# Kernel optimization log

Measured on AMD Instinct MI355X. Metric: run time of the kernel, lower is better.

## Reference

```python
import jax, jax.numpy as jnp
import numpy as np

NUM_ANCHORS = 3
NUM_CLASS = 7
IMG_SIZE = 608.0


def setup_inputs() -> dict:
    key = jax.random.key(0)
    k1, k2 = jax.random.split(key)
    B, A, G = 32, NUM_ANCHORS, 152
    C = 7 + NUM_CLASS  # per-anchor channels
    x = jax.random.normal(k1, (B, A * C, G, G), dtype=jnp.float32)
    # anchor (w, h) priors in pixels
    anchors = jnp.array([[38.0, 84.0], [110.0, 45.0], [170.0, 160.0]], dtype=jnp.float32)
    return {"x": x, "anchors": anchors}


def _decode(x, anchors):
    B, AC, G, _ = x.shape
    A = NUM_ANCHORS
    C = AC // A  # 14
    # [B, A, G, G, C]
    y = x.reshape(B, A, C, G, G).transpose(0, 1, 3, 4, 2)

    off_x = jax.nn.sigmoid(y[..., 0])
    off_y = jax.nn.sigmoid(y[..., 1])
    scale_w = jnp.exp(y[..., 2])
    scale_h = jnp.exp(y[..., 3])
    im = y[..., 4]
    re = y[..., 5]
    conf = jax.nn.sigmoid(y[..., 6])
    cls = y[..., 7:]  # [B, A, G, G, num_class]

    # grid_x[gy, gx] = gx ; grid_y = grid_x.T
    grid = jnp.arange(G, dtype=jnp.float32)
    grid_x = grid[None, :]  # broadcasts over rows
    grid_y = grid[:, None]
    stride = IMG_SIZE / G

    anchor_x = jnp.floor((off_x + grid_x) * stride)
    anchor_y = jnp.floor((off_y + grid_y) * stride)
    anchor_yaw = jnp.arctan(im / re)
    anchor_w = scale_w * anchors[None, :, 0, None, None]
    anchor_h = scale_h * anchors[None, :, 1, None, None]

    # classes: [B, A, G, G, nc] -> [B, A, nc, G, G] -> [B, A*nc, G, G]
    cls_flat = cls.transpose(0, 1, 4, 2, 3).reshape(B, A * NUM_CLASS, G, G)

    # channel concat exactly as torch.cat(..., dim=1): 8 fields of A channels + A*nc class channels
    feats = jnp.concatenate(
        [im, re, anchor_yaw, conf, anchor_x, anchor_y, anchor_w, anchor_h, cls_flat],
        axis=1,
    )  # [B, 15*A, G, G]
    # faithful to .view(B, 15, A, G, G).permute(0, 2, 3, 4, 1).view(B, A*G*G, 15)
    pred = feats.reshape(B, 15, A, G, G).transpose(0, 2, 3, 4, 1).reshape(B, A * G * G, 15)
    return pred


def reference(x, anchors):
    return _decode(x, anchors)
```

## Files before the change

kernel.cpp:

```cpp
#include <hip/hip_runtime.h>


constexpr int G   = 152;
constexpr int GG  = G * G;
constexpr int Cc  = 14;
constexpr int NTHREADS  = 256;
constexpr int TILE_ROWS = 1024;

typedef float f32x4 __attribute__((ext_vector_type(4)));

__device__ __forceinline__ float sigmoidf_(float v) {
    return 1.0f / (1.0f + __expf(-v));
}

__global__ __launch_bounds__(NTHREADS) void decode_kernel(
    const float* __restrict__ x, const float* __restrict__ anchors,
    float* __restrict__ out, int total_rows)
{
    __shared__ f32x4 lds4[TILE_ROWS * 15 / 4];

    const int t  = threadIdx.x;
    const int r0 = blockIdx.x * TILE_ROWS + t * 4;

    if (r0 + 3 < total_rows) {
        const unsigned ba = (unsigned)r0 / (unsigned)GG;
        const int s0      = r0 - (int)ba * GG;
        const unsigned b  = ba / 3u;
        const int a2      = (int)(ba - b * 3u);
        const int gy      = s0 / G;
        const int gx0     = s0 - gy * G;

        const float an_w = anchors[a2 * 2 + 0];
        const float an_h = anchors[a2 * 2 + 1];

        const float* xb = x + (size_t)(b * 42u) * GG + s0;
        const int cb = a2 * Cc;

        const f32x4 vtx = *(const f32x4*)(xb + (size_t)(cb + 0) * GG);
        const f32x4 vty = *(const f32x4*)(xb + (size_t)(cb + 1) * GG);
        const f32x4 vtw = *(const f32x4*)(xb + (size_t)(cb + 2) * GG);
        const f32x4 vth = *(const f32x4*)(xb + (size_t)(cb + 3) * GG);
        const f32x4 vim = *(const f32x4*)(xb + (size_t)(cb + 4) * GG);
        const f32x4 vre = *(const f32x4*)(xb + (size_t)(cb + 5) * GG);
        const f32x4 vcf = *(const f32x4*)(xb + (size_t)(cb + 6) * GG);
        f32x4 vcls[7];
#pragma unroll
        for (int fc = 0; fc < 7; ++fc) {
            const int cc = fc * 3 + a2;
            const int as = cc / 7;
            const int k  = cc - as * 7;
            vcls[fc] = *(const f32x4*)(xb + (size_t)(as * Cc + 7 + k) * GG);
        }

        float v[60];
#pragma unroll
        for (int u = 0; u < 4; ++u) {
            const float im  = vim[u];
            const float re  = vre[u];
            const float yaw = atanf(im / re);
            const float cf  = sigmoidf_(vcf[u]);
            const float ax  = floorf((sigmoidf_(vtx[u]) + (float)(gx0 + u)) * 4.0f);
            const float ay  = floorf((sigmoidf_(vty[u]) + (float)gy) * 4.0f);
            const float aw  = __expf(vtw[u]) * an_w;
            const float ah  = __expf(vth[u]) * an_h;
            v[u * 15 + 0] = im;  v[u * 15 + 1] = re;
            v[u * 15 + 2] = yaw; v[u * 15 + 3] = cf;
            v[u * 15 + 4] = ax;  v[u * 15 + 5] = ay;
            v[u * 15 + 6] = aw;  v[u * 15 + 7] = ah;
#pragma unroll
            for (int fc = 0; fc < 7; ++fc) v[u * 15 + 8 + fc] = vcls[fc][u];
        }
#pragma unroll
        for (int j = 0; j < 15; ++j) {
            f32x4 q = { v[4 * j], v[4 * j + 1], v[4 * j + 2], v[4 * j + 3] };
            lds4[15 * t + j] = q;
        }
    }
    __syncthreads();

    const long long block_word0 = (long long)blockIdx.x * (TILE_ROWS * 15);
    const long long total_words = (long long)total_rows * 15;
    float* outp = out + block_word0;
#pragma unroll
    for (int i = 0; i < 15; ++i) {
        const int gr = i * NTHREADS + t;
        if (block_word0 + 4 * gr + 3 < total_words) {
            f32x4 q = lds4[gr];
            *(f32x4*)(outp + 4 * gr) = q;
        }
    }
}

extern "C" void kernel_launch(void* const* d_in, const int* in_sizes, int n_in,
                              void* d_out, int out_size, void* d_ws, size_t ws_size,
                              hipStream_t stream) {
    const float* x       = (const float*)d_in[0];
    const float* anchors = (const float*)d_in[1];
    float* out           = (float*)d_out;

    const int B          = in_sizes[0] / (3 * Cc * GG);
    const int total_rows = B * 3 * GG;
    const int nblocks    = (total_rows + TILE_ROWS - 1) / TILE_ROWS;

    hipLaunchKernelGGL(decode_kernel, dim3(nblocks), dim3(NTHREADS), 0, stream,
                       x, anchors, out, total_rows);
}
```

Baseline: 43.59 us.

## Process one row per thread with per-wave LDS staging and wave barrier

Each thread now handles one output row with scalar loads instead of four rows with vector loads. Each wave writes its own 240-float4 slice of a smaller LDS tile and syncs with a wave barrier instead of a block barrier. Launch bounds ask for 8 blocks per SM, and bounds checks are dropped on the assumption that total rows divide evenly by 256. The aim is higher occupancy and less block-level synchronisation, at the cost of narrower global loads and many more blocks.

```diff
diff --git a/kernel.cpp b/kernel.cpp
--- a/kernel.cpp
+++ b/kernel.cpp
@@ -4,8 +4,7 @@
 constexpr int G   = 152;
 constexpr int GG  = G * G;
 constexpr int Cc  = 14;
-constexpr int NTHREADS  = 256;
-constexpr int TILE_ROWS = 1024;
+constexpr int NTHREADS = 256;
 
 typedef float f32x4 __attribute__((ext_vector_type(4)));
 
@@ -13,78 +12,67 @@
     return 1.0f / (1.0f + __expf(-v));
 }
 
-__global__ __launch_bounds__(NTHREADS) void decode_kernel(
+__global__ __launch_bounds__(NTHREADS, 8) void decode_kernel(
     const float* __restrict__ x, const float* __restrict__ anchors,
-    float* __restrict__ out, int total_rows)
+    float* __restrict__ out)
 {
-    __shared__ f32x4 lds4[TILE_ROWS * 15 / 4];
+    __shared__ f32x4 lds4[NTHREADS * 15 / 4];
+    float* ldsf = (float*)lds4;
 
-    const int t  = threadIdx.x;
-    const int r0 = blockIdx.x * TILE_ROWS + t * 4;
+    const int t = threadIdx.x;
+    const int w = t >> 6;
+    const int l = t & 63;
+    const int r = blockIdx.x * NTHREADS + t;
 
-    if (r0 + 3 < total_rows) {
-        const unsigned ba = (unsigned)r0 / (unsigned)GG;
-        const int s0      = r0 - (int)ba * GG;
-        const unsigned b  = ba / 3u;
-        const int a2      = (int)(ba - b * 3u);
-        const int gy      = s0 / G;
-        const int gx0     = s0 - gy * G;
+    const unsigned ba = (unsigned)r / (unsigned)GG;
+    const int s       = r - (int)ba * GG;
+    const unsigned b  = ba / 3u;
+    const int a2      = (int)(ba - b * 3u);
+    const int gy      = s / G;
+    const int gx      = s - gy * G;
 
-        const float an_w = anchors[a2 * 2 + 0];
-        const float an_h = anchors[a2 * 2 + 1];
+    const float an_w = anchors[a2 * 2 + 0];
+    const float an_h = anchors[a2 * 2 + 1];
 
-        const float* xb = x + (size_t)(b * 42u) * GG + s0;
-        const int cb = a2 * Cc;
+    const float* xb = x + (size_t)(b * 42u) * GG + s;
+    const int cb = a2 * Cc;
 
-        const f32x4 vtx = *(const f32x4*)(xb + (size_t)(cb + 0) * GG);
-        const f32x4 vty = *(const f32x4*)(xb + (size_t)(cb + 1) * GG);
-        const f32x4 vtw = *(const f32x4*)(xb + (size_t)(cb + 2) * GG);
-        const f32x4 vth = *(const f32x4*)(xb + (size_t)(cb + 3) * GG);
-        const f32x4 vim = *(const f32x4*)(xb + (size_t)(cb + 4) * GG);
-        const f32x4 vre = *(const f32x4*)(xb + (size_t)(cb + 5) * GG);
-        const f32x4 vcf = *(const f32x4*)(xb + (size_t)(cb + 6) * GG);
-        f32x4 vcls[7];
+    const float tx = xb[(size_t)(cb + 0) * GG];
+    const float ty = xb[(size_t)(cb + 1) * GG];
+    const float tw = xb[(size_t)(cb + 2) * GG];
+    const float th = xb[(size_t)(cb + 3) * GG];
+    const float im = xb[(size_t)(cb + 4) * GG];
+    const float re = xb[(size_t)(cb + 5) * GG];
+    const float cf = xb[(size_t)(cb + 6) * GG];
+    float cls[7];
 #pragma unroll
-        for (int fc = 0; fc < 7; ++fc) {
-            const int cc = fc * 3 + a2;
-            const int as = cc / 7;
-            const int k  = cc - as * 7;
-            vcls[fc] = *(const f32x4*)(xb + (size_t)(as * Cc + 7 + k) * GG);
-        }
+    for (int fc = 0; fc < 7; ++fc) {
+        const int cc = fc * 3 + a2;
+        const int as = cc / 7;
+        const int k  = cc - as * 7;
+        cls[fc] = xb[(size_t)(as * Cc + 7 + k) * GG];
+    }
 
-        float v[60];
+    float* wb = ldsf + 15 * t;
+    wb[0] = im;
+    wb[1] = re;
+    wb[2] = atanf(im / re);
+    wb[3] = sigmoidf_(cf);
+    wb[4] = floorf((sigmoidf_(tx) + (float)gx) * 4.0f);
+    wb[5] = floorf((sigmoidf_(ty) + (float)gy) * 4.0f);
+    wb[6] = __expf(tw) * an_w;
+    wb[7] = __expf(th) * an_h;
 #pragma unroll
-        for (int u = 0; u < 4; ++u) {
-            const float im  = vim[u];
-            const float re  = vre[u];
-            const float yaw = atanf(im / re);
-            const float cf  = sigmoidf_(vcf[u]);
-            const float ax  = floorf((sigmoidf_(vtx[u]) + (float)(gx0 + u)) * 4.0f);
-            const float ay  = floorf((sigmoidf_(vty[u]) + (float)gy) * 4.0f);
-            const float aw  = __expf(vtw[u]) * an_w;
-            const float ah  = __expf(vth[u]) * an_h;
-            v[u * 15 + 0] = im;  v[u * 15 + 1] = re;
-            v[u * 15 + 2] = yaw; v[u * 15 + 3] = cf;
-            v[u * 15 + 4] = ax;  v[u * 15 + 5] = ay;
-            v[u * 15 + 6] = aw;  v[u * 15 + 7] = ah;
+    for (int fc = 0; fc < 7; ++fc) wb[8 + fc] = cls[fc];
+
+    __builtin_amdgcn_wave_barrier();
+
+    float* outp = out + (long long)blockIdx.x * (NTHREADS * 15);
 #pragma unroll
-            for (int fc = 0; fc < 7; ++fc) v[u * 15 + 8 + fc] = vcls[fc][u];
-        }
-#pragma unroll
-        for (int j = 0; j < 15; ++j) {
-            f32x4 q = { v[4 * j], v[4 * j + 1], v[4 * j + 2], v[4 * j + 3] };
-            lds4[15 * t + j] = q;
-        }
-    }
-    __syncthreads();
-
-    const long long block_word0 = (long long)blockIdx.x * (TILE_ROWS * 15);
-    const long long total_words = (long long)total_rows * 15;
-    float* outp = out + block_word0;
-#pragma unroll
-    for (int i = 0; i < 15; ++i) {
-        const int gr = i * NTHREADS + t;
-        if (block_word0 + 4 * gr + 3 < total_words) {
+    for (int i = 0; i < 4; ++i) {
+        const int idx = 64 * i + l;
+        if (idx < 240) {
+            const int gr = 240 * w + idx;
             f32x4 q = lds4[gr];
             *(f32x4*)(outp + 4 * gr) = q;
         }
@@ -100,8 +88,8 @@
 
     const int B          = in_sizes[0] / (3 * Cc * GG);
     const int total_rows = B * 3 * GG;
-    const int nblocks    = (total_rows + TILE_ROWS - 1) / TILE_ROWS;
+    const int nblocks    = total_rows / NTHREADS;
 
     hipLaunchKernelGGL(decode_kernel, dim3(nblocks), dim3(NTHREADS), 0, stream,
-                       x, anchors, out, total_rows);
+                       x, anchors, out);
 }
```

Result: faster. 42.06 us (-3.5%).
